# Optimization experiments

Hardware: AMD Instinct MI355X
Metric: run time of the kernel (lower is better)

The kernel has to match this reference:

```python
import jax, jax.numpy as jnp
import numpy as np

EMBED = 1024
HEADS = 16
HEAD_DIM = EMBED // HEADS
CAUSAL = True
NUM_SEQS = 8
SEQ = 1024
TOTAL = NUM_SEQS * SEQ


def setup_inputs() -> dict:
    key = jax.random.key(0)
    ks = jax.random.split(key, 8)
    s = 0.02
    return {
        "hidden_states": jax.random.normal(ks[0], (TOTAL, EMBED), dtype=jnp.float32),
        "seq_len": jnp.full((NUM_SEQS,), SEQ, dtype=jnp.int64),
        "Wq": jax.random.normal(ks[1], (EMBED, EMBED), dtype=jnp.float32) * s,
        "bq": jnp.zeros((EMBED,), dtype=jnp.float32),
        "Wk": jax.random.normal(ks[2], (EMBED, EMBED), dtype=jnp.float32) * s,
        "Wv": jax.random.normal(ks[3], (EMBED, EMBED), dtype=jnp.float32) * s,
        "bv": jnp.zeros((EMBED,), dtype=jnp.float32),
        "Wo": jax.random.normal(ks[4], (EMBED, EMBED), dtype=jnp.float32) * s,
        "bo": jnp.zeros((EMBED,), dtype=jnp.float32),
    }


def _varlen_attention(q, k, v, seq_len):
    # q,k,v: [T, H, D] packed ragged tokens; seq_len: static per-sequence lengths.
    # Equivalent to the per-sequence Python loop, but done as one padded batch.
    sl = np.asarray(seq_len)
    B = sl.shape[0]
    S = int(sl.max())
    cu = np.concatenate([[0], np.cumsum(sl)])  # cu_seqlens
    pos = np.arange(S)
    # gather indices [B, S] (clipped inside each segment; invalid masked below)
    idx = cu[:-1, None] + np.minimum(pos[None, :], sl[:, None] - 1)
    valid = pos[None, :] < sl[:, None]  # [B, S]
    qp, kp, vp = q[idx], k[idx], v[idx]  # [B, S, H, D]
    scale = 1.0 / np.float32(np.sqrt(q.shape[-1]))
    scores = jnp.einsum('bqhd,bkhd->bhqk', qp, kp) * scale  # [B, H, S, S]
    mask = valid[:, None, None, :]  # valid keys
    if CAUSAL:
        mask = mask & (pos[None, :] <= pos[:, None])[None, None, :, :]
    scores = jnp.where(mask, scores, -jnp.inf)
    probs = jax.nn.softmax(scores, axis=-1)
    out = jnp.einsum('bhqk,bkhd->bqhd', probs, vp)  # [B, S, H, D]
    # unpad back to packed layout [T, H*D]
    b_of = np.repeat(np.arange(B), sl)
    p_of = np.concatenate([np.arange(l) for l in sl])
    return out[b_of, p_of].reshape(q.shape[0], -1)


def reference(hidden_states, seq_len, Wq, bq, Wk, Wv, bv, Wo, bo):
    T = hidden_states.shape[0]
    q = (hidden_states @ Wq.T + bq).reshape(T, HEADS, HEAD_DIM)
    k = (hidden_states @ Wk.T).reshape(T, HEADS, HEAD_DIM)  # k_proj has no bias
    v = (hidden_states @ Wv.T + bv).reshape(T, HEADS, HEAD_DIM)
    attn = _varlen_attention(q, k, v, seq_len)  # [T, EMBED]
    return attn @ Wo.T + bo
```

## Files before the change

kernel.cpp:

```cpp
#include <hip/hip_runtime.h>
#include <hip/hip_bf16.h>


typedef unsigned short u16;
typedef unsigned int   u32;
typedef __attribute__((ext_vector_type(8))) short bf16x8;
typedef __attribute__((ext_vector_type(4))) float f32x4;
typedef __attribute__((ext_vector_type(16))) float f32x16;
typedef __attribute__((ext_vector_type(4))) u32 u32x4;

#define AS1 __attribute__((address_space(1)))
#define AS3 __attribute__((address_space(3)))
#define FENCE asm volatile("" ::: "memory")
#define BAR() do { FENCE; __builtin_amdgcn_s_barrier(); FENCE; } while (0)

__device__ __forceinline__ u16 f2bf(float f) {
  u32 x = __float_as_uint(f);
  x += 0x7fffu + ((x >> 16) & 1u);
  return (u16)(x >> 16);
}
__device__ __forceinline__ u32 pk2(float a, float b) {
  return (u32)f2bf(a) | ((u32)f2bf(b) << 16);
}

__global__ __launch_bounds__(256) void cvt_all(const float* __restrict__ hs,
                                               const float* __restrict__ Wq,
                                               const float* __restrict__ Wk,
                                               const float* __restrict__ Wv,
                                               const float* __restrict__ Wo,
                                               const float* __restrict__ bq,
                                               const float* __restrict__ bv,
                                               u16* __restrict__ Xb,
                                               u16* __restrict__ Wqkv,
                                               u16* __restrict__ Wob,
                                               float* __restrict__ bias) {
  if (blockIdx.x == gridDim.x - 1) {
    for (int i = threadIdx.x; i < 3072; i += 256) {
      float v = 0.f;
      if (i < 1024) v = bq[i];
      else if (i >= 2048) v = bv[i - 2048];
      bias[i] = v;
    }
  }
  int i = blockIdx.x * 256 + threadIdx.x;
  const int stride = gridDim.x * 256;
  for (; i < 3145728; i += stride) {
    const float* src;
    u16* dst;
    int off;
    if (i < 2097152) {
      src = hs; dst = Xb; off = i;
    } else {
      int j = i - 2097152;
      int m = j >> 18;
      off = j & 262143;
      src = (m == 0) ? Wq : (m == 1) ? Wk : (m == 2) ? Wv : Wo;
      dst = (m < 3) ? (Wqkv + (size_t)m * 1048576) : Wob;
    }
    float4 v = ((const float4*)src)[off];
    u32 lo = (u32)f2bf(v.x) | ((u32)f2bf(v.y) << 16);
    u32 hi = (u32)f2bf(v.z) | ((u32)f2bf(v.w) << 16);
    ((u32*)dst)[off * 2]     = lo;
    ((u32*)dst)[off * 2 + 1] = hi;
  }
}

__device__ __forceinline__ void quad16(f32x4 (&acc)[4][2],
                                       const bf16x8 (&af)[4][2],
                                       const bf16x8 (&bf)[2][2]) {
#pragma unroll
  for (int m = 0; m < 4; ++m)
#pragma unroll
    for (int n = 0; n < 2; ++n)
#pragma unroll
      for (int kk = 0; kk < 2; ++kk)
        acc[m][n] = __builtin_amdgcn_mfma_f32_16x16x32_bf16(
            af[m][kk], bf[n][kk], acc[m][n], 0, 0, 0);
}

template <int OUT_MODE>
__global__ __launch_bounds__(512, 2) void gemm8p(const u16* __restrict__ A,
                                                 const u16* __restrict__ Bw,
                                                 const float* __restrict__ bias,
                                                 void* __restrict__ C,
                                                 int M, int N, int K, int nbn) {
  __shared__ __align__(16) u16 sA[2][2][128 * 64];
  __shared__ __align__(16) u16 sB[2][2][128 * 64];

  const int cpx = gridDim.x >> 3;
  const int swz = ((int)blockIdx.x & 7) * cpx + ((int)blockIdx.x >> 3);
  const int bn = swz % nbn, bm = swz / nbn;
  const int tid = threadIdx.x;
  const int l = tid & 63, w = tid >> 6;
  const int l15 = l & 15, lg = (l >> 4) & 3;
  const int wr = w >> 2, wc = w & 3;
  const int bh = wc >> 1;

  const u16* Ab = A + (size_t)(bm * 256) * K;
  const u16* Bb = Bw + (size_t)(bn * 256) * K;

  const int sr = w * 8 + (l >> 3);
  const int sch = (l & 7) ^ ((l >> 3) & 7);
  const int sldso = w * 64 * 8;

  auto STAGE = [&](const u16* Xb, u16* lds, int hf, int kt) {
    const u16* src = Xb + (size_t)(hf * 128) * K + kt * 64;
#pragma unroll
    for (int j = 0; j < 2; ++j)
      __builtin_amdgcn_global_load_lds(
          (const AS1 void*)(src + (size_t)(j * 64 + sr) * K + sch * 8),
          (AS3 void*)((AS3 u16*)lds + j * 512 * 8 + sldso), 16, 0, 0);
  };
  auto LDA = [&](const u16* Ah, int mh, int m, int kk) -> bf16x8 {
    int row = mh * 64 + m * 16 + l15;
    int ch = (kk * 4 + lg) ^ (l15 & 7);
    return *(const bf16x8*)&Ah[row * 64 + ch * 8];
  };
  auto LDB = [&](const u16* Bh, int nh, int n, int kk) -> bf16x8 {
    int row = (wc & 1) * 64 + nh * 32 + n * 16 + l15;
    int ch = (kk * 4 + lg) ^ (l15 & 7);
    return *(const bf16x8*)&Bh[row * 64 + ch * 8];
  };

  f32x4 acc[2][2][4][2] = {};
  const int NT = K >> 6;

  STAGE(Ab, &sA[0][0][0], 0, 0);
  STAGE(Ab, &sA[0][1][0], 1, 0);
  STAGE(Bb, &sB[0][0][0], 0, 0);
  STAGE(Bb, &sB[0][1][0], 1, 0);
  STAGE(Bb, &sB[1][0][0], 0, 1);
  STAGE(Bb, &sB[1][1][0], 1, 1);
  asm volatile("s_waitcnt vmcnt(4)" ::: "memory");
  BAR();

  for (int kt = 0; kt < NT; ++kt) {
    const int p = kt & 1;
    const u16* Ah = &sA[p][wr][0];
    const u16* Bh = &sB[p][bh][0];
    bf16x8 af0[4][2], af1[4][2], bf0[2][2], bf1[2][2];

#pragma unroll
    for (int m = 0; m < 4; ++m)
#pragma unroll
      for (int kk = 0; kk < 2; ++kk) af0[m][kk] = LDA(Ah, 0, m, kk);
#pragma unroll
    for (int n = 0; n < 2; ++n)
#pragma unroll
      for (int kk = 0; kk < 2; ++kk) bf0[n][kk] = LDB(Bh, 0, n, kk);
    if (kt + 1 < NT) STAGE(Ab, &sA[p ^ 1][0][0], 0, kt + 1);
    BAR();
    __builtin_amdgcn_s_setprio(1);
    quad16(acc[0][0], af0, bf0);
    __builtin_amdgcn_s_setprio(0);
    BAR();

#pragma unroll
    for (int n = 0; n < 2; ++n)
#pragma unroll
      for (int kk = 0; kk < 2; ++kk) bf1[n][kk] = LDB(Bh, 1, n, kk);
    if (kt + 1 < NT) STAGE(Ab, &sA[p ^ 1][1][0], 1, kt + 1);
    BAR();
    __builtin_amdgcn_s_setprio(1);
    quad16(acc[0][1], af0, bf1);
    __builtin_amdgcn_s_setprio(0);
    BAR();

#pragma unroll
    for (int m = 0; m < 4; ++m)
#pragma unroll
      for (int kk = 0; kk < 2; ++kk) af1[m][kk] = LDA(Ah, 1, m, kk);
    if (kt + 2 < NT) STAGE(Bb, &sB[p][0][0], 0, kt + 2);
    BAR();
    __builtin_amdgcn_s_setprio(1);
    quad16(acc[1][1], af1, bf1);
    __builtin_amdgcn_s_setprio(0);
    BAR();

    if (kt + 2 < NT) STAGE(Bb, &sB[p][1][0], 1, kt + 2);
    BAR();
    __builtin_amdgcn_s_setprio(1);
    quad16(acc[1][0], af1, bf0);
    __builtin_amdgcn_s_setprio(0);
    if (kt >= NT - 2) asm volatile("s_waitcnt vmcnt(0)" ::: "memory");
    else              asm volatile("s_waitcnt vmcnt(4)" ::: "memory");
    BAR();
  }

#pragma unroll
  for (int mh = 0; mh < 2; ++mh)
#pragma unroll
    for (int m = 0; m < 4; ++m)
#pragma unroll
      for (int i = 0; i < 4; ++i) {
        int row = bm * 256 + wr * 128 + mh * 64 + m * 16 + lg * 4 + i;
#pragma unroll
        for (int nh = 0; nh < 2; ++nh)
#pragma unroll
          for (int n = 0; n < 2; ++n) {
            int col = bn * 256 + wc * 64 + nh * 32 + n * 16 + l15;
            float v = acc[mh][nh][m][n][i] + bias[col];
            if (OUT_MODE == 0)
              ((u16*)C)[(size_t)row * N + col] = f2bf(v);
            else
              ((float*)C)[(size_t)row * N + col] = v;
          }
      }
}

__global__ __launch_bounds__(256, 4) void attn_kernel(const u16* __restrict__ qkv,
                                                      u16* __restrict__ attnout) {
  const int bid = (blockIdx.x & 7) * 128 + (blockIdx.x >> 3);
  const int qb = 7 - (bid & 7);
  const int h = (bid >> 3) & 15;
  const int s = bid >> 7;
  const int tid = threadIdx.x;
  const int l = tid & 63, w = tid >> 6;
  const int l31 = l & 31;
  const int hi = l >> 5;
  const int pb = (l >> 3) & 1;

  __shared__ __align__(16) u16 Ks[128 * 64];
  __shared__ __align__(16) u32 Vt2[64 * 65];

  const u16* kbase = qkv + (size_t)(s * 1024) * 3072 + 1024 + h * 64;
  const u16* vbase = qkv + (size_t)(s * 1024) * 3072 + 2048 + h * 64;

  bf16x8 qf[4];
  {
    const u16* qptr = qkv + (size_t)(s * 1024 + qb * 128 + w * 32 + l31) * 3072 + h * 64 + hi * 8;
#pragma unroll
    for (int c = 0; c < 4; ++c) qf[c] = *(const bf16x8*)(qptr + c * 16);
  }

  float m_r = -1e30f, l_r = 0.f;
  f32x16 o0 = {}, o1 = {};

  const int nt = qb + 1;

  const int vkv = w * 8 + (l >> 3);
  const int vd0 = (l & 7) * 8;
  const int vkp = w * 4 + (l >> 4);
  const int dEff = vd0 + pb * 4;

  const int srow = w * 8 + (l >> 3);
  const int schunk = (l & 7) ^ ((l >> 3) & 7);

  bf16x8 vcur[4], vnx[4];
#pragma unroll
  for (int p = 0; p < 4; ++p)
    vcur[p] = *(const bf16x8*)(vbase + (size_t)(p * 32 + vkv) * 3072 + vd0);

  for (int t = 0; t < nt; ++t) {
    const u16* kt = kbase + (size_t)(t * 128) * 3072;
#pragma unroll
    for (int p = 0; p < 4; ++p)
      __builtin_amdgcn_global_load_lds(
          (const AS1 void*)(kt + (size_t)(p * 32 + srow) * 3072 + schunk * 8),
          (AS3 void*)((AS3 u16*)Ks + p * 2048 + w * 512), 16, 0, 0);

#pragma unroll
    for (int p = 0; p < 4; ++p) {
      u32 dw0 = ((u32*)&vcur[p])[0], dw1 = ((u32*)&vcur[p])[1];
      u32 dw2 = ((u32*)&vcur[p])[2], dw3 = ((u32*)&vcur[p])[3];
      u32 s0 = (u32)__shfl_xor((int)(pb ? dw0 : dw2), 8, 64);
      u32 s1 = (u32)__shfl_xor((int)(pb ? dw1 : dw3), 8, 64);
      u32 md0 = pb ? dw2 : dw0, md1 = pb ? dw3 : dw1;
      u32 lo0 = pb ? s0 : md0, hi0 = pb ? md0 : s0;
      u32 lo1 = pb ? s1 : md1, hi1 = pb ? md1 : s1;
      int kp = p * 16 + vkp;
      Vt2[(dEff + 0) * 65 + kp] = (lo0 & 0xffffu) | (hi0 << 16);
      Vt2[(dEff + 1) * 65 + kp] = (lo0 >> 16) | (hi0 & 0xffff0000u);
      Vt2[(dEff + 2) * 65 + kp] = (lo1 & 0xffffu) | (hi1 << 16);
      Vt2[(dEff + 3) * 65 + kp] = (lo1 >> 16) | (hi1 & 0xffff0000u);
    }
    __syncthreads();

    if (t + 1 < nt) {
      const u16* vt = vbase + (size_t)((t + 1) * 128) * 3072;
#pragma unroll
      for (int p = 0; p < 4; ++p)
        vnx[p] = *(const bf16x8*)(vt + (size_t)(p * 32 + vkv) * 3072 + vd0);
    }

    const bool diag = (t == nt - 1);
#pragma unroll
    for (int sub = 0; sub < 4; ++sub) {
      if (!(diag && sub > w)) {
        f32x16 sc = {};
#pragma unroll
        for (int c = 0; c < 4; ++c) {
          int r = sub * 32 + l31;
          int pc = (2 * c + hi) ^ (l31 & 7);
          bf16x8 kf = *(const bf16x8*)&Ks[r * 64 + pc * 8];
          sc = __builtin_amdgcn_mfma_f32_32x32x16_bf16(kf, qf[c], sc, 0, 0, 0);
        }
        float tv[16];
#pragma unroll
        for (int r = 0; r < 16; ++r) tv[r] = sc[r] * 0.125f;
        if (diag && sub == w) {
#pragma unroll
          for (int r = 0; r < 16; ++r) {
            int kvloc = (r & 3) + 8 * (r >> 2) + 4 * hi;
            if (kvloc > l31) tv[r] = -1e30f;
          }
        }
        float t0 = fmaxf(fmaxf(tv[0], tv[1]), fmaxf(tv[2], tv[3]));
        float t1 = fmaxf(fmaxf(tv[4], tv[5]), fmaxf(tv[6], tv[7]));
        float t2 = fmaxf(fmaxf(tv[8], tv[9]), fmaxf(tv[10], tv[11]));
        float t3 = fmaxf(fmaxf(tv[12], tv[13]), fmaxf(tv[14], tv[15]));
        float tmax = fmaxf(fmaxf(t0, t1), fmaxf(t2, t3));
        tmax = fmaxf(tmax, __shfl_xor(tmax, 32, 64));
        if (!__all(tmax <= m_r + 8.0f)) {
          float nm = fmaxf(m_r, tmax);
          float alpha = __expf(m_r - nm);
          m_r = nm;
          l_r *= alpha;
#pragma unroll
          for (int r = 0; r < 16; ++r) { o0[r] *= alpha; o1[r] *= alpha; }
        }
#pragma unroll
        for (int r = 0; r < 16; ++r) tv[r] = __expf(tv[r] - m_r);
        float s0_ = (tv[0] + tv[1]) + (tv[2] + tv[3]);
        float s1_ = (tv[4] + tv[5]) + (tv[6] + tv[7]);
        float s2_ = (tv[8] + tv[9]) + (tv[10] + tv[11]);
        float s3_ = (tv[12] + tv[13]) + (tv[14] + tv[15]);
        float psum = (s0_ + s1_) + (s2_ + s3_);
        psum += __shfl_xor(psum, 32, 64);
        l_r += psum;
#pragma unroll
        for (int s01 = 0; s01 < 2; ++s01) {
          u32 W0 = pk2(tv[8 * s01 + 0], tv[8 * s01 + 1]);
          u32 W1 = pk2(tv[8 * s01 + 2], tv[8 * s01 + 3]);
          u32 X0 = pk2(tv[8 * s01 + 4], tv[8 * s01 + 5]);
          u32 X1 = pk2(tv[8 * s01 + 6], tv[8 * s01 + 7]);
          u32 rW0 = (u32)__shfl_xor((int)W0, 32, 64);
          u32 rW1 = (u32)__shfl_xor((int)W1, 32, 64);
          u32 rX0 = (u32)__shfl_xor((int)X0, 32, 64);
          u32 rX1 = (u32)__shfl_xor((int)X1, 32, 64);
          u32x4 av;
          av[0] = hi ? rX0 : W0;
          av[1] = hi ? rX1 : W1;
          av[2] = hi ? X0 : rW0;
          av[3] = hi ? X1 : rW1;
          bf16x8 pa = *(bf16x8*)&av;
          int kpb = sub * 16 + s01 * 8 + hi * 4;
          u32x4 v0 = *(const u32x4*)&Vt2[(size_t)l31 * 65 + kpb];
          o0 = __builtin_amdgcn_mfma_f32_32x32x16_bf16(pa, *(bf16x8*)&v0, o0, 0, 0, 0);
          u32x4 v1 = *(const u32x4*)&Vt2[(size_t)(32 + l31) * 65 + kpb];
          o1 = __builtin_amdgcn_mfma_f32_32x32x16_bf16(pa, *(bf16x8*)&v1, o1, 0, 0, 0);
        }
      }
    }
    __syncthreads();
#pragma unroll
    for (int p = 0; p < 4; ++p) vcur[p] = vnx[p];
  }

#pragma unroll
  for (int r = 0; r < 16; ++r) {
    int qp = (r & 3) + 8 * (r >> 2) + 4 * hi;
    float ls = __shfl(l_r, qp, 64);
    float inv = __builtin_amdgcn_rcpf(ls);
    int trow = s * 1024 + qb * 128 + w * 32 + qp;
    attnout[(size_t)trow * 1024 + h * 64 + l31]      = f2bf(o0[r] * inv);
    attnout[(size_t)trow * 1024 + h * 64 + 32 + l31] = f2bf(o1[r] * inv);
  }
}

extern "C" void kernel_launch(void* const* d_in, const int* in_sizes, int n_in,
                              void* d_out, int out_size, void* d_ws, size_t ws_size,
                              hipStream_t stream) {
  const float* hs = (const float*)d_in[0];
  const float* Wq = (const float*)d_in[2];
  const float* bq = (const float*)d_in[3];
  const float* Wk = (const float*)d_in[4];
  const float* Wv = (const float*)d_in[5];
  const float* bv = (const float*)d_in[6];
  const float* Wo = (const float*)d_in[7];
  const float* bo = (const float*)d_in[8];

  char* ws = (char*)d_ws;
  u16* Xb    = (u16*)ws;
  u16* Wqkv  = (u16*)(ws + 16777216);
  u16* Wob   = (u16*)(ws + 23068672);
  float* bqk = (float*)(ws + 25165824);
  u16* qkv   = (u16*)(ws + 25178112);
  u16* attn  = (u16*)(ws + 75509760);

  cvt_all<<<2048, 256, 0, stream>>>(hs, Wq, Wk, Wv, Wo, bq, bv, Xb, Wqkv, Wob, bqk);

  gemm8p<0><<<384, 512, 0, stream>>>(Xb, Wqkv, bqk, qkv, 8192, 3072, 1024, 12);

  attn_kernel<<<1024, 256, 0, stream>>>(qkv, attn);

  gemm8p<1><<<128, 512, 0, stream>>>(attn, Wob, bo, d_out, 8192, 1024, 1024, 4);
}
```

Before: 264.0 us.

## Shrink GEMM tile to 128x256 with triple-buffered B and LDS-staged epilogue

Each GEMM block now covers a 128x256 tile instead of 256x256, which doubles the grid size (768 and 256 blocks) so more blocks are available to fill the CUs. The B operand rotates through a three-stage ring buffer while A stays double-buffered, and each k-step now has two MFMA phases instead of four. The epilogue writes the accumulators to LDS and then issues vectorized, coalesced global stores with the bias added. In exchange each block reuses its loaded tiles less, uses 128 KB of LDS, and the epilogue adds extra barriers.

```diff
diff --git a/kernel.cpp b/kernel.cpp
--- a/kernel.cpp
+++ b/kernel.cpp
@@ -8,6 +8,7 @@
 typedef __attribute__((ext_vector_type(4))) float f32x4;
 typedef __attribute__((ext_vector_type(16))) float f32x16;
 typedef __attribute__((ext_vector_type(4))) u32 u32x4;
+typedef __attribute__((ext_vector_type(2))) u32 u32x2;
 
 #define AS1 __attribute__((address_space(1)))
 #define AS3 __attribute__((address_space(3)))
@@ -65,27 +66,15 @@
   }
 }
 
-__device__ __forceinline__ void quad16(f32x4 (&acc)[4][2],
-                                       const bf16x8 (&af)[4][2],
-                                       const bf16x8 (&bf)[2][2]) {
-#pragma unroll
-  for (int m = 0; m < 4; ++m)
-#pragma unroll
-    for (int n = 0; n < 2; ++n)
-#pragma unroll
-      for (int kk = 0; kk < 2; ++kk)
-        acc[m][n] = __builtin_amdgcn_mfma_f32_16x16x32_bf16(
-            af[m][kk], bf[n][kk], acc[m][n], 0, 0, 0);
-}
-
 template <int OUT_MODE>
 __global__ __launch_bounds__(512, 2) void gemm8p(const u16* __restrict__ A,
                                                  const u16* __restrict__ Bw,
                                                  const float* __restrict__ bias,
                                                  void* __restrict__ C,
                                                  int M, int N, int K, int nbn) {
-  __shared__ __align__(16) u16 sA[2][2][128 * 64];
-  __shared__ __align__(16) u16 sB[2][2][128 * 64];
+  __shared__ __align__(16) unsigned char smem[131072];
+  auto bufA = [&](int p) -> u16* { return (u16*)(smem + (size_t)p * 16384); };
+  auto bufB = [&](int p) -> u16* { return (u16*)(smem + 32768 + (size_t)p * 32768); };
 
   const int cpx = gridDim.x >> 3;
   const int swz = ((int)blockIdx.x & 7) * cpx + ((int)blockIdx.x >> 3);
@@ -94,118 +83,132 @@
   const int l = tid & 63, w = tid >> 6;
   const int l15 = l & 15, lg = (l >> 4) & 3;
   const int wr = w >> 2, wc = w & 3;
-  const int bh = wc >> 1;
-
-  const u16* Ab = A + (size_t)(bm * 256) * K;
+
+  const u16* Ab = A + (size_t)(bm * 128) * K;
   const u16* Bb = Bw + (size_t)(bn * 256) * K;
 
   const int sr = w * 8 + (l >> 3);
   const int sch = (l & 7) ^ ((l >> 3) & 7);
   const int sldso = w * 64 * 8;
 
-  auto STAGE = [&](const u16* Xb, u16* lds, int hf, int kt) {
-    const u16* src = Xb + (size_t)(hf * 128) * K + kt * 64;
+  auto STG = [&](const u16* src, u16* lds) {
 #pragma unroll
     for (int j = 0; j < 2; ++j)
       __builtin_amdgcn_global_load_lds(
           (const AS1 void*)(src + (size_t)(j * 64 + sr) * K + sch * 8),
-          (AS3 void*)((AS3 u16*)lds + j * 512 * 8 + sldso), 16, 0, 0);
+          (AS3 void*)((AS3 u16*)lds + j * 4096 + sldso), 16, 0, 0);
   };
-  auto LDA = [&](const u16* Ah, int mh, int m, int kk) -> bf16x8 {
-    int row = mh * 64 + m * 16 + l15;
+  auto LDA = [&](const u16* Ah, int m, int kk) -> bf16x8 {
+    int row = wr * 64 + m * 16 + l15;
     int ch = (kk * 4 + lg) ^ (l15 & 7);
     return *(const bf16x8*)&Ah[row * 64 + ch * 8];
   };
-  auto LDB = [&](const u16* Bh, int nh, int n, int kk) -> bf16x8 {
-    int row = (wc & 1) * 64 + nh * 32 + n * 16 + l15;
+  auto LDB = [&](const u16* Bh, int n, int kk) -> bf16x8 {
+    int row = wc * 64 + n * 16 + l15;
     int ch = (kk * 4 + lg) ^ (l15 & 7);
     return *(const bf16x8*)&Bh[row * 64 + ch * 8];
   };
 
-  f32x4 acc[2][2][4][2] = {};
+  f32x4 acc[4][4] = {};
   const int NT = K >> 6;
 
-  STAGE(Ab, &sA[0][0][0], 0, 0);
-  STAGE(Ab, &sA[0][1][0], 1, 0);
-  STAGE(Bb, &sB[0][0][0], 0, 0);
-  STAGE(Bb, &sB[0][1][0], 1, 0);
-  STAGE(Bb, &sB[1][0][0], 0, 1);
-  STAGE(Bb, &sB[1][1][0], 1, 1);
+  STG(Ab, bufA(0));
+  STG(Bb, bufB(0));
+  STG(Bb + (size_t)128 * K, bufB(0) + 8192);
+  STG(Bb + 64, bufB(1));
+  STG(Bb + (size_t)128 * K + 64, bufB(1) + 8192);
   asm volatile("s_waitcnt vmcnt(4)" ::: "memory");
   BAR();
 
+  int pa = 0, pb = 0;
   for (int kt = 0; kt < NT; ++kt) {
-    const int p = kt & 1;
-    const u16* Ah = &sA[p][wr][0];
-    const u16* Bh = &sB[p][bh][0];
-    bf16x8 af0[4][2], af1[4][2], bf0[2][2], bf1[2][2];
+    const u16* Ah = bufA(pa);
+    const u16* Bh = bufB(pb);
+    const int pa1 = pa ^ 1;
+    int pb2 = pb + 2; if (pb2 >= 3) pb2 -= 3;
+    bf16x8 af[4][2], bf0[2][2], bf1[2][2];
 
 #pragma unroll
     for (int m = 0; m < 4; ++m)
 #pragma unroll
-      for (int kk = 0; kk < 2; ++kk) af0[m][kk] = LDA(Ah, 0, m, kk);
+      for (int kk = 0; kk < 2; ++kk) af[m][kk] = LDA(Ah, m, kk);
 #pragma unroll
     for (int n = 0; n < 2; ++n)
 #pragma unroll
-      for (int kk = 0; kk < 2; ++kk) bf0[n][kk] = LDB(Bh, 0, n, kk);
-    if (kt + 1 < NT) STAGE(Ab, &sA[p ^ 1][0][0], 0, kt + 1);
+      for (int kk = 0; kk < 2; ++kk) bf0[n][kk] = LDB(Bh, n, kk);
+    if (kt + 1 < NT) STG(Ab + (kt + 1) * 64, bufA(pa1));
+    if (kt + 2 < NT) STG(Bb + (kt + 2) * 64, bufB(pb2));
     BAR();
     __builtin_amdgcn_s_setprio(1);
-    quad16(acc[0][0], af0, bf0);
+#pragma unroll
+    for (int m = 0; m < 4; ++m)
+#pragma unroll
+      for (int n = 0; n < 2; ++n)
+#pragma unroll
+        for (int kk = 0; kk < 2; ++kk)
+          acc[m][n] = __builtin_amdgcn_mfma_f32_16x16x32_bf16(
+              af[m][kk], bf0[n][kk], acc[m][n], 0, 0, 0);
     __builtin_amdgcn_s_setprio(0);
     BAR();
 
 #pragma unroll
     for (int n = 0; n < 2; ++n)
 #pragma unroll
-      for (int kk = 0; kk < 2; ++kk) bf1[n][kk] = LDB(Bh, 1, n, kk);
-    if (kt + 1 < NT) STAGE(Ab, &sA[p ^ 1][1][0], 1, kt + 1);
+      for (int kk = 0; kk < 2; ++kk) bf1[n][kk] = LDB(Bh, n + 2, kk);
+    if (kt + 2 < NT) STG(Bb + (size_t)128 * K + (kt + 2) * 64, bufB(pb2) + 8192);
     BAR();
     __builtin_amdgcn_s_setprio(1);
-    quad16(acc[0][1], af0, bf1);
+#pragma unroll
+    for (int m = 0; m < 4; ++m)
+#pragma unroll
+      for (int n = 0; n < 2; ++n)
+#pragma unroll
+        for (int kk = 0; kk < 2; ++kk)
+          acc[m][n + 2] = __builtin_amdgcn_mfma_f32_16x16x32_bf16(
+              af[m][kk], bf1[n][kk], acc[m][n + 2], 0, 0, 0);
     __builtin_amdgcn_s_setprio(0);
+    if (kt < NT - 2) asm volatile("s_waitcnt vmcnt(4)" ::: "memory");
+    else             asm volatile("s_waitcnt vmcnt(0)" ::: "memory");
     BAR();
-
-#pragma unroll
-    for (int m = 0; m < 4; ++m)
-#pragma unroll
-      for (int kk = 0; kk < 2; ++kk) af1[m][kk] = LDA(Ah, 1, m, kk);
-    if (kt + 2 < NT) STAGE(Bb, &sB[p][0][0], 0, kt + 2);
-    BAR();
-    __builtin_amdgcn_s_setprio(1);
-    quad16(acc[1][1], af1, bf1);
-    __builtin_amdgcn_s_setprio(0);
-    BAR();
-
-    if (kt + 2 < NT) STAGE(Bb, &sB[p][1][0], 1, kt + 2);
-    BAR();
-    __builtin_amdgcn_s_setprio(1);
-    quad16(acc[1][0], af1, bf0);
-    __builtin_amdgcn_s_setprio(0);
-    if (kt >= NT - 2) asm volatile("s_waitcnt vmcnt(0)" ::: "memory");
-    else              asm volatile("s_waitcnt vmcnt(4)" ::: "memory");
-    BAR();
-  }
-
-#pragma unroll
-  for (int mh = 0; mh < 2; ++mh)
-#pragma unroll
-    for (int m = 0; m < 4; ++m)
-#pragma unroll
-      for (int i = 0; i < 4; ++i) {
-        int row = bm * 256 + wr * 128 + mh * 64 + m * 16 + lg * 4 + i;
-#pragma unroll
-        for (int nh = 0; nh < 2; ++nh)
-#pragma unroll
-          for (int n = 0; n < 2; ++n) {
-            int col = bn * 256 + wc * 64 + nh * 32 + n * 16 + l15;
-            float v = acc[mh][nh][m][n][i] + bias[col];
-            if (OUT_MODE == 0)
-              ((u16*)C)[(size_t)row * N + col] = f2bf(v);
-            else
-              ((float*)C)[(size_t)row * N + col] = v;
-          }
+    pa = pa1;
+    pb = (pb + 1 == 3) ? 0 : pb + 1;
+  }
+
+  float* eb = (float*)smem;
+  const int mychunk = wc >> 1;
+#pragma unroll
+  for (int ch = 0; ch < 2; ++ch) {
+    __syncthreads();
+    if (mychunk == ch) {
+#pragma unroll
+      for (int m = 0; m < 4; ++m)
+#pragma unroll
+        for (int n = 0; n < 4; ++n)
+#pragma unroll
+          for (int i = 0; i < 4; ++i)
+            eb[(wr * 64 + m * 16 + lg * 4 + i) * 132 + (wc & 1) * 64 + n * 16 + l15] =
+                acc[m][n][i];
+    }
+    __syncthreads();
+#pragma unroll
+    for (int ps = 0; ps < 8; ++ps) {
+      int idx = (ps * 512 + tid) * 4;
+      int row = idx >> 7, col = idx & 127;
+      f32x4 v = *(const f32x4*)&eb[row * 132 + col];
+      int colg = bn * 256 + ch * 128 + col;
+      f32x4 b = *(const f32x4*)&bias[colg];
+      size_t go = (size_t)(bm * 128 + row) * N + colg;
+      if (OUT_MODE == 0) {
+        u32x2 o;
+        o[0] = pk2(v[0] + b[0], v[1] + b[1]);
+        o[1] = pk2(v[2] + b[2], v[3] + b[3]);
+        *(u32x2*)((u16*)C + go) = o;
+      } else {
+        f32x4 o = {v[0] + b[0], v[1] + b[1], v[2] + b[2], v[3] + b[3]};
+        *(f32x4*)((float*)C + go) = o;
       }
+    }
+  }
 }
 
 __global__ __launch_bounds__(256, 4) void attn_kernel(const u16* __restrict__ qkv,
@@ -390,9 +393,9 @@
 
   cvt_all<<<2048, 256, 0, stream>>>(hs, Wq, Wk, Wv, Wo, bq, bv, Xb, Wqkv, Wob, bqk);
 
-  gemm8p<0><<<384, 512, 0, stream>>>(Xb, Wqkv, bqk, qkv, 8192, 3072, 1024, 12);
+  gemm8p<0><<<768, 512, 0, stream>>>(Xb, Wqkv, bqk, qkv, 8192, 3072, 1024, 12);
 
   attn_kernel<<<1024, 256, 0, stream>>>(qkv, attn);
 
-  gemm8p<1><<<128, 512, 0, stream>>>(attn, Wob, bo, d_out, 8192, 1024, 1024, 4);
-}
+  gemm8p<1><<<256, 512, 0, stream>>>(attn, Wob, bo, d_out, 8192, 1024, 1024, 4);
+}
```

Result: faster. 252.4 us (-4.4%).
